# Kernel optimization log

Measured on AMD Instinct MI355X. Metric: run time of the kernel, lower is better.

Reference implementation:

```python
import jax, jax.numpy as jnp
import numpy as np

D_MODEL = 256
N_HEADS = 8
N_LEVELS = 3
N_POINTS = 4
HEAD_DIM = D_MODEL // N_HEADS
SPATIAL_SHAPES = [(80, 80), (40, 40), (20, 20)]
B = 16
LEN_Q = 300
N_TOTAL = sum(h * w for h, w in SPATIAL_SHAPES)  # 8400
N_LP = N_LEVELS * N_POINTS


def setup_inputs() -> dict:
    key = jax.random.key(0)
    ks = jax.random.split(key, 8)
    s = 0.02
    return {
        "query": jax.random.normal(ks[0], (B, LEN_Q, D_MODEL), jnp.float32),
        "reference_points": jax.random.uniform(ks[1], (B, LEN_Q, N_LEVELS, 2), jnp.float32),
        "input_flatten": jax.random.normal(ks[2], (B, N_TOTAL, D_MODEL), jnp.float32),
        "W_off": jax.random.normal(ks[3], (D_MODEL, N_HEADS * N_LP * 2), jnp.float32) * s,
        "b_off": jnp.zeros((N_HEADS * N_LP * 2,), jnp.float32),
        "W_attn": jax.random.normal(ks[4], (D_MODEL, N_HEADS * N_LP), jnp.float32) * s,
        "b_attn": jnp.zeros((N_HEADS * N_LP,), jnp.float32),
        "W_val": jax.random.normal(ks[5], (D_MODEL, D_MODEL), jnp.float32) * s,
        "b_val": jnp.zeros((D_MODEL,), jnp.float32),
        "W_out": jax.random.normal(ks[6], (D_MODEL, D_MODEL), jnp.float32) * s,
        "b_out": jnp.zeros((D_MODEL,), jnp.float32),
    }


def _ms_deform_core(value, sampling_locations, attention_weights):
    # value: (B, n_heads, head_dim, N_total); locations: (B, Lq, H, L, P, 2) in [0,1]
    Bq, Lq = sampling_locations.shape[0], sampling_locations.shape[1]
    BN = Bq * N_HEADS
    grids = 2.0 * sampling_locations - 1.0
    starts = np.cumsum([0] + [h * w for h, w in SPATIAL_SHAPES])
    sampled_levels = []
    for lid, (H, W) in enumerate(SPATIAL_SHAPES):
        val_l = value[..., starts[lid]:starts[lid + 1]]                    # (B,H,hd,HW)
        val_flat = val_l.reshape(BN, HEAD_DIM, H * W).transpose(0, 2, 1)   # (BN,HW,hd)
        g = grids[:, :, :, lid].transpose(0, 2, 1, 3, 4).reshape(BN, Lq, N_POINTS, 2)
        ix = ((g[..., 0] + 1.0) * W - 1.0) / 2.0
        iy = ((g[..., 1] + 1.0) * H - 1.0) / 2.0
        ix0 = jnp.floor(ix).astype(jnp.int32)
        iy0 = jnp.floor(iy).astype(jnp.int32)
        ix1 = ix0 + 1
        iy1 = iy0 + 1
        fx = (ix - ix0.astype(ix.dtype))[..., None]
        fy = (iy - iy0.astype(iy.dtype))[..., None]

        def corner(iyc, ixc):
            valid = ((ixc >= 0) & (ixc < W) & (iyc >= 0) & (iyc < H)).astype(val_flat.dtype)
            idx = (jnp.clip(iyc, 0, H - 1) * W + jnp.clip(ixc, 0, W - 1))
            idx = idx.reshape(BN, Lq * N_POINTS, 1)
            v = jnp.take_along_axis(val_flat, idx, axis=1)
            return v.reshape(BN, Lq, N_POINTS, HEAD_DIM) * valid[..., None]

        v00 = corner(iy0, ix0)
        v01 = corner(iy0, ix1)
        v10 = corner(iy1, ix0)
        v11 = corner(iy1, ix1)
        sampled = ((1 - fx) * (1 - fy)) * v00 + (fx * (1 - fy)) * v01 \
                + ((1 - fx) * fy) * v10 + (fx * fy) * v11
        sampled_levels.append(sampled.transpose(0, 3, 1, 2))               # (BN,hd,Lq,P)
    sv = jnp.stack(sampled_levels, axis=-2).reshape(BN, HEAD_DIM, Lq, N_LP)
    a = attention_weights.transpose(0, 2, 1, 3).reshape(BN, 1, Lq, N_LP)
    out = jnp.sum(sv * a, axis=-1)                                         # (BN,hd,Lq)
    return out.reshape(Bq, D_MODEL, Lq).transpose(0, 2, 1)                 # (B,Lq,D)


def reference(query, reference_points, input_flatten,
              W_off, b_off, W_attn, b_attn, W_val, b_val, W_out, b_out):
    Bq, Lq = query.shape[0], query.shape[1]
    value = input_flatten @ W_val + b_val
    value = value.reshape(Bq, -1, N_HEADS, HEAD_DIM).transpose(0, 2, 3, 1)  # (B,H,hd,N)
    off = (query @ W_off + b_off).reshape(Bq, Lq, N_HEADS, N_LEVELS, N_POINTS, 2)
    attn = jax.nn.softmax((query @ W_attn + b_attn).reshape(Bq, Lq, N_HEADS, N_LP), axis=-1)
    # offset normalizer is (W,H) per level (x first)
    norm = jnp.array([[w, h] for h, w in SPATIAL_SHAPES], jnp.float32)
    loc = reference_points[:, :, None, :, None, :] + off / norm[None, None, None, :, None, :]
    out = _ms_deform_core(value, loc, attn)
    return out @ W_out + b_out
```

## Files before the change

### kernel.cpp

```cpp
#include <hip/hip_runtime.h>
#include <hip/hip_bf16.h>

#define DM 256
#define NH 8
#define HD 32
#define NLV 3
#define NPT 4
#define NLP 12
#define BB 16
#define LQ 300
#define NT 8400
#define MROWS (BB * NT)
#define QROWS (BB * LQ)
#define KP2 72

typedef __bf16 bf16x8 __attribute__((ext_vector_type(8)));
typedef float  f32x16 __attribute__((ext_vector_type(16)));

__global__ void k_wt(const float* __restrict__ W_val,
                     const float* __restrict__ W_off,
                     const float* __restrict__ W_attn,
                     const float* __restrict__ W_out,
                     __hip_bfloat16* __restrict__ Wf,
                     __hip_bfloat16* __restrict__ Wf2,
                     __hip_bfloat16* __restrict__ Wf3)
{
    const int n = blockIdx.x;
    const int k = threadIdx.x;
    if (n < 256) {
        Wf[(size_t)(k >> 3) * 2048 + n * 8 + (k & 7)] =
            __float2bfloat16(W_val[(size_t)k * 256 + n]);
    } else if (n < 544) {
        const int n2 = n - 256;
        float v = (n2 < 192) ? W_off[(size_t)k * 192 + n2]
                             : W_attn[(size_t)k * 96 + (n2 - 192)];
        Wf2[(size_t)(k >> 3) * 2304 + n2 * 8 + (k & 7)] = __float2bfloat16(v);
    } else {
        const int n3 = n - 544;
        Wf3[(size_t)(k >> 3) * 2048 + n3 * 8 + (k & 7)] =
            __float2bfloat16(W_out[(size_t)k * 256 + n3]);
    }
}

__global__ __launch_bounds__(256) void k_mm1(
    const float* __restrict__ A,
    const __hip_bfloat16* __restrict__ Wf,
    const float* __restrict__ bval,
    __hip_bfloat16* __restrict__ V,
    const float* __restrict__ Q,
    const __hip_bfloat16* __restrict__ Wf2,
    const float* __restrict__ boff,
    const float* __restrict__ battn,
    float* __restrict__ off_out,
    float* __restrict__ attn_out)
{
    __shared__ __hip_bfloat16 As[2][32 * KP2];

    const int t    = threadIdx.x;
    const int wave = t >> 6;
    const int lane = t & 63;
    const int lm   = lane & 31;
    const int kh   = lane >> 5;
    const int lk   = kh * 8;
    const int ar   = t >> 3;
    const int ak   = (t & 7) * 8;

    if (blockIdx.x < MROWS / 32) {
        const int m0 = blockIdx.x * 32;

        f32x16 acc[2];
#pragma unroll
        for (int j = 0; j < 2; j++)
#pragma unroll
            for (int e = 0; e < 16; e++) acc[j][e] = 0.f;

        const __hip_bfloat16* wf0 = Wf + (size_t)(wave * 64 + lm) * 8 + kh * 2048;

        {
            const float* ap = A + (size_t)(m0 + ar) * 256 + ak;
            float4 a0 = *(const float4*)ap;
            float4 a1 = *(const float4*)(ap + 4);
            union { __hip_bfloat162 h2[4]; bf16x8 v; } ua;
            ua.h2[0] = __float22bfloat162_rn(make_float2(a0.x, a0.y));
            ua.h2[1] = __float22bfloat162_rn(make_float2(a0.z, a0.w));
            ua.h2[2] = __float22bfloat162_rn(make_float2(a1.x, a1.y));
            ua.h2[3] = __float22bfloat162_rn(make_float2(a1.z, a1.w));
            *(bf16x8*)(&As[0][ar * KP2 + ak]) = ua.v;
        }
        __syncthreads();

#pragma unroll
        for (int it = 0; it < 4; ++it) {
            const int buf = it & 1;
            float4 na0, na1;
            if (it < 3) {
                const float* ap = A + (size_t)(m0 + ar) * 256 + (it + 1) * 64 + ak;
                na0 = *(const float4*)ap;
                na1 = *(const float4*)(ap + 4);
            }
#pragma unroll
            for (int ks = 0; ks < 4; ++ks) {
                const int g = it * 4 + ks;
                bf16x8 af = *(const bf16x8*)(&As[buf][lm * KP2 + ks * 16 + lk]);
                bf16x8 b0 = *(const bf16x8*)(wf0 + (size_t)g * 4096);
                bf16x8 b1 = *(const bf16x8*)(wf0 + (size_t)g * 4096 + 256);
                acc[0] = __builtin_amdgcn_mfma_f32_32x32x16_bf16(af, b0, acc[0], 0, 0, 0);
                acc[1] = __builtin_amdgcn_mfma_f32_32x32x16_bf16(af, b1, acc[1], 0, 0, 0);
            }
            if (it < 3) {
                union { __hip_bfloat162 h2[4]; bf16x8 v; } ua;
                ua.h2[0] = __float22bfloat162_rn(make_float2(na0.x, na0.y));
                ua.h2[1] = __float22bfloat162_rn(make_float2(na0.z, na0.w));
                ua.h2[2] = __float22bfloat162_rn(make_float2(na1.x, na1.y));
                ua.h2[3] = __float22bfloat162_rn(make_float2(na1.z, na1.w));
                *(bf16x8*)(&As[buf ^ 1][ar * KP2 + ak]) = ua.v;
                __syncthreads();
            }
        }

#pragma unroll
        for (int j = 0; j < 2; j++) {
            const int n  = wave * 64 + j * 32 + lm;
            const float bn = bval[n];
            const int h  = n >> 5;
            const int d  = n & 31;
#pragma unroll
            for (int r = 0; r < 16; r++) {
                int rl = (r & 3) + 8 * (r >> 2) + 4 * kh;
                int m  = m0 + rl;
                int b  = m / NT;
                int pos = m - b * NT;
                V[((size_t)(b * NH + h) * NT + pos) * HD + d] =
                    __float2bfloat16(acc[j][r] + bn);
            }
        }
    } else {
        const int m0 = (blockIdx.x - MROWS / 32) * 32;

        f32x16 acc[3];
#pragma unroll
        for (int j = 0; j < 3; j++)
#pragma unroll
            for (int e = 0; e < 16; e++) acc[j][e] = 0.f;

        const __hip_bfloat16* wf0 = Wf2 + (size_t)(wave * 96 + lm) * 8 + kh * 2304;

        {
            const float* ap = Q + (size_t)(m0 + ar) * 256 + ak;
            float4 a0 = *(const float4*)ap;
            float4 a1 = *(const float4*)(ap + 4);
            union { __hip_bfloat162 h2[4]; bf16x8 v; } ua;
            ua.h2[0] = __float22bfloat162_rn(make_float2(a0.x, a0.y));
            ua.h2[1] = __float22bfloat162_rn(make_float2(a0.z, a0.w));
            ua.h2[2] = __float22bfloat162_rn(make_float2(a1.x, a1.y));
            ua.h2[3] = __float22bfloat162_rn(make_float2(a1.z, a1.w));
            *(bf16x8*)(&As[0][ar * KP2 + ak]) = ua.v;
        }
        __syncthreads();

#pragma unroll
        for (int it = 0; it < 4; ++it) {
            const int buf = it & 1;
            float4 na0, na1;
            if (it < 3) {
                const float* ap = Q + (size_t)(m0 + ar) * 256 + (it + 1) * 64 + ak;
                na0 = *(const float4*)ap;
                na1 = *(const float4*)(ap + 4);
            }
#pragma unroll
            for (int ks = 0; ks < 4; ++ks) {
                const int g = it * 4 + ks;
                bf16x8 af = *(const bf16x8*)(&As[buf][lm * KP2 + ks * 16 + lk]);
                if (wave < 3) {
#pragma unroll
                    for (int j = 0; j < 3; j++) {
                        bf16x8 bf = *(const bf16x8*)(wf0 + (size_t)g * 4608 + j * 256);
                        acc[j] = __builtin_amdgcn_mfma_f32_32x32x16_bf16(af, bf, acc[j], 0, 0, 0);
                    }
                }
            }
            if (it < 3) {
                union { __hip_bfloat162 h2[4]; bf16x8 v; } ua;
                ua.h2[0] = __float22bfloat162_rn(make_float2(na0.x, na0.y));
                ua.h2[1] = __float22bfloat162_rn(make_float2(na0.z, na0.w));
                ua.h2[2] = __float22bfloat162_rn(make_float2(na1.x, na1.y));
                ua.h2[3] = __float22bfloat162_rn(make_float2(na1.z, na1.w));
                *(bf16x8*)(&As[buf ^ 1][ar * KP2 + ak]) = ua.v;
                __syncthreads();
            }
        }

        if (wave < 3) {
#pragma unroll
            for (int j = 0; j < 3; j++) {
                const int n = wave * 96 + j * 32 + lm;
                const float bias_ = (n < 192) ? boff[n] : battn[n - 192];
#pragma unroll
                for (int r = 0; r < 16; r++) {
                    int rl = (r & 3) + 8 * (r >> 2) + 4 * kh;
                    int m  = m0 + rl;
                    float v = acc[j][r] + bias_;
                    if (n < 192) off_out[(size_t)m * 192 + n] = v;
                    else         attn_out[(size_t)m * 96 + (n - 192)] = v;
                }
            }
        }
    }
}

__global__ __launch_bounds__(256) void k_sample(
    const float* __restrict__ off_raw,
    const float* __restrict__ attn_raw,
    const float* __restrict__ refp,
    const __hip_bfloat16* __restrict__ V,
    __hip_bfloat16* __restrict__ sampled)
{
    const int t  = threadIdx.x;
    const int q2 = t >> 7;
    const int tq = t & 127;

    const int bid  = blockIdx.x;
    const int xcd  = bid & 7;
    const int slot = bid >> 3;
    const int hi   = (slot >= 150) ? 1 : 0;
    const int b    = xcd + (hi << 3);
    const int bq   = b * LQ + (slot - hi * 150) * 2 + q2;

    __shared__ float aw[2][96];
    __shared__ float wc[2][96][4];
    __shared__ int   ic[2][96][4];

    if (tq < 8) {
        float v[12];
        float mx = -1e30f;
#pragma unroll
        for (int i = 0; i < 12; i++) {
            v[i] = attn_raw[(size_t)bq * 96 + tq * 12 + i];
            mx = fmaxf(mx, v[i]);
        }
        float s = 0.f;
#pragma unroll
        for (int i = 0; i < 12; i++) { v[i] = expf(v[i] - mx); s += v[i]; }
        float inv = 1.f / s;
#pragma unroll
        for (int i = 0; i < 12; i++) aw[q2][tq * 12 + i] = v[i] * inv;
    }
    __syncthreads();

    if (tq < 96) {
        const float dims[3]  = {80.f, 40.f, 20.f};
        const int startsl[3] = {0, 6400, 8000};
        const int idiml[3]   = {80, 40, 20};
        int h = tq / 12, lp = tq - h * 12, l = lp >> 2, p = lp & 3;
        float ox = off_raw[(size_t)bq * 192 + ((h * 3 + l) * 4 + p) * 2 + 0];
        float oy = off_raw[(size_t)bq * 192 + ((h * 3 + l) * 4 + p) * 2 + 1];
        float rx = refp[(size_t)bq * 6 + l * 2 + 0];
        float ry = refp[(size_t)bq * 6 + l * 2 + 1];
        float D  = dims[l];
        float lx = rx + ox / D;
        float ly = ry + oy / D;
        float ix = lx * D - 0.5f;
        float iy = ly * D - 0.5f;
        const int Dl = idiml[l];
        const int st = startsl[l];

        float fix = floorf(ix), fiy = floorf(iy);
        int ix0 = (int)fix, iy0 = (int)fiy;
        int ix1 = ix0 + 1, iy1 = iy0 + 1;
        float fx = ix - fix, fy = iy - fiy;

        float mx0 = (ix0 >= 0 && ix0 < Dl) ? 1.f : 0.f;
        float mx1 = (ix1 >= 0 && ix1 < Dl) ? 1.f : 0.f;
        float my0 = (iy0 >= 0 && iy0 < Dl) ? 1.f : 0.f;
        float my1 = (iy1 >= 0 && iy1 < Dl) ? 1.f : 0.f;

        int cx0 = min(max(ix0, 0), Dl - 1);
        int cx1 = min(max(ix1, 0), Dl - 1);
        int cy0 = min(max(iy0, 0), Dl - 1);
        int cy1 = min(max(iy1, 0), Dl - 1);

        float a = aw[q2][tq];
        wc[q2][tq][0] = (1.f - fx) * (1.f - fy) * mx0 * my0 * a;
        wc[q2][tq][1] = fx * (1.f - fy) * mx1 * my0 * a;
        wc[q2][tq][2] = (1.f - fx) * fy * mx0 * my1 * a;
        wc[q2][tq][3] = fx * fy * mx1 * my1 * a;
        ic[q2][tq][0] = (st + cy0 * Dl + cx0) * HD;
        ic[q2][tq][1] = (st + cy0 * Dl + cx1) * HD;
        ic[q2][tq][2] = (st + cy1 * Dl + cx0) * HD;
        ic[q2][tq][3] = (st + cy1 * Dl + cx1) * HD;
    }
    __syncthreads();

    const int h  = tq >> 4;
    const int dp = (tq & 15) * 2;
    const __hip_bfloat16* vb = V + (size_t)(b * NH + h) * NT * HD + dp;

    float acc0 = 0.f, acc1 = 0.f;
#pragma unroll
    for (int lp = 0; lp < 12; lp++) {
        const int s = h * 12 + lp;
        float4 w4 = *(const float4*)(&wc[q2][s][0]);
        int4   i4 = *(const int4*)(&ic[q2][s][0]);
        float2 v00 = __bfloat1622float2(*(const __hip_bfloat162*)(vb + i4.x));
        float2 v01 = __bfloat1622float2(*(const __hip_bfloat162*)(vb + i4.y));
        float2 v10 = __bfloat1622float2(*(const __hip_bfloat162*)(vb + i4.z));
        float2 v11 = __bfloat1622float2(*(const __hip_bfloat162*)(vb + i4.w));
        acc0 = fmaf(w4.x, v00.x, fmaf(w4.y, v01.x, fmaf(w4.z, v10.x, fmaf(w4.w, v11.x, acc0))));
        acc1 = fmaf(w4.x, v00.y, fmaf(w4.y, v01.y, fmaf(w4.z, v10.y, fmaf(w4.w, v11.y, acc1))));
    }
    *(__hip_bfloat162*)(sampled + (size_t)bq * 256 + h * 32 + dp) =
        __float22bfloat162_rn(make_float2(acc0, acc1));
}

__global__ __launch_bounds__(256) void k_outproj(
    const __hip_bfloat16* __restrict__ A,
    const __hip_bfloat16* __restrict__ Wf3,
    const float* __restrict__ bias,
    float* __restrict__ out)
{
    __shared__ __hip_bfloat16 As[2][32 * KP2];

    const int t    = threadIdx.x;
    const int m0   = blockIdx.x * 32;
    const int wave = t >> 6;
    const int lane = t & 63;
    const int lm   = lane & 31;
    const int kh   = lane >> 5;
    const int lk   = kh * 8;
    const int ar   = t >> 3;
    const int ak   = (t & 7) * 8;

    f32x16 acc[2];
#pragma unroll
    for (int j = 0; j < 2; j++)
#pragma unroll
        for (int e = 0; e < 16; e++) acc[j][e] = 0.f;

    const __hip_bfloat16* wf0 = Wf3 + (size_t)(wave * 64 + lm) * 8 + kh * 2048;

    *(bf16x8*)(&As[0][ar * KP2 + ak]) =
        *(const bf16x8*)(A + (size_t)(m0 + ar) * 256 + ak);
    __syncthreads();

#pragma unroll
    for (int it = 0; it < 4; ++it) {
        const int buf = it & 1;
        bf16x8 na;
        if (it < 3)
            na = *(const bf16x8*)(A + (size_t)(m0 + ar) * 256 + (it + 1) * 64 + ak);
#pragma unroll
        for (int ks = 0; ks < 4; ++ks) {
            const int g = it * 4 + ks;
            bf16x8 af = *(const bf16x8*)(&As[buf][lm * KP2 + ks * 16 + lk]);
            bf16x8 b0 = *(const bf16x8*)(wf0 + (size_t)g * 4096);
            bf16x8 b1 = *(const bf16x8*)(wf0 + (size_t)g * 4096 + 256);
            acc[0] = __builtin_amdgcn_mfma_f32_32x32x16_bf16(af, b0, acc[0], 0, 0, 0);
            acc[1] = __builtin_amdgcn_mfma_f32_32x32x16_bf16(af, b1, acc[1], 0, 0, 0);
        }
        if (it < 3) {
            *(bf16x8*)(&As[buf ^ 1][ar * KP2 + ak]) = na;
            __syncthreads();
        }
    }

#pragma unroll
    for (int j = 0; j < 2; j++) {
        const int n = wave * 64 + j * 32 + lm;
        const float bn = bias[n];
#pragma unroll
        for (int r = 0; r < 16; r++) {
            int rl = (r & 3) + 8 * (r >> 2) + 4 * kh;
            int m  = m0 + rl;
            out[(size_t)m * 256 + n] = acc[j][r] + bn;
        }
    }
}

extern "C" void kernel_launch(void* const* d_in, const int* in_sizes, int n_in,
                              void* d_out, int out_size, void* d_ws, size_t ws_size,
                              hipStream_t stream) {
    const float* query  = (const float*)d_in[0];
    const float* refp   = (const float*)d_in[1];
    const float* inputf = (const float*)d_in[2];
    const float* W_off  = (const float*)d_in[3];
    const float* b_off  = (const float*)d_in[4];
    const float* W_attn = (const float*)d_in[5];
    const float* b_attn = (const float*)d_in[6];
    const float* W_val  = (const float*)d_in[7];
    const float* b_val  = (const float*)d_in[8];
    const float* W_out  = (const float*)d_in[9];
    const float* b_out  = (const float*)d_in[10];
    float* out = (float*)d_out;

    char* ws = (char*)d_ws;
    __hip_bfloat16* value   = (__hip_bfloat16*)ws;
    float* off_raw          = (float*)(ws + 68812800);
    float* attn_raw         = (float*)(ws + 72499200);
    __hip_bfloat16* sampled = (__hip_bfloat16*)(ws + 74342400);
    __hip_bfloat16* Wf      = (__hip_bfloat16*)(ws + 76800000);
    __hip_bfloat16* Wf2     = (__hip_bfloat16*)(ws + 76931072);
    __hip_bfloat16* Wf3     = (__hip_bfloat16*)(ws + 77078528);

    k_wt<<<800, 256, 0, stream>>>(W_val, W_off, W_attn, W_out, Wf, Wf2, Wf3);
    k_mm1<<<MROWS / 32 + QROWS / 32, 256, 0, stream>>>(
        inputf, Wf, b_val, value, query, Wf2, b_off, b_attn, off_raw, attn_raw);
    k_sample<<<QROWS / 2, 256, 0, stream>>>(off_raw, attn_raw, refp, value, sampled);
    k_outproj<<<QROWS / 32, 256, 0, stream>>>(sampled, Wf3, b_out, out);
}
```

Baseline: 267.4 us.

## Drop LDS staging in GEMMs; load MFMA operands directly with register prefetch

Reworks the three MFMA GEMM kernels so each wave loads its A and weight fragments straight from global memory into registers, using a 4-deep (or 2-deep) rotating prefetch. This removes the shared-memory double buffer and its __syncthreads. Weights are now stored row-major (n, k) to match the per-lane fragment loads, and the idle fourth wave in the query projection now exits early. The cost is that each of the four waves loads the same A tile separately (4x redundant A reads, served from L1/L2), uses more registers, and issues strided row loads for A.

```diff
diff --git a/kernel.cpp b/kernel.cpp
--- a/kernel.cpp
+++ b/kernel.cpp
@@ -12,7 +12,6 @@
 #define NT 8400
 #define MROWS (BB * NT)
 #define QROWS (BB * LQ)
-#define KP2 72
 
 typedef __bf16 bf16x8 __attribute__((ext_vector_type(8)));
 typedef float  f32x16 __attribute__((ext_vector_type(16)));
@@ -28,17 +27,15 @@
     const int n = blockIdx.x;
     const int k = threadIdx.x;
     if (n < 256) {
-        Wf[(size_t)(k >> 3) * 2048 + n * 8 + (k & 7)] =
-            __float2bfloat16(W_val[(size_t)k * 256 + n]);
+        Wf[(size_t)n * 256 + k] = __float2bfloat16(W_val[(size_t)k * 256 + n]);
     } else if (n < 544) {
         const int n2 = n - 256;
         float v = (n2 < 192) ? W_off[(size_t)k * 192 + n2]
                              : W_attn[(size_t)k * 96 + (n2 - 192)];
-        Wf2[(size_t)(k >> 3) * 2304 + n2 * 8 + (k & 7)] = __float2bfloat16(v);
+        Wf2[(size_t)n2 * 256 + k] = __float2bfloat16(v);
     } else {
         const int n3 = n - 544;
-        Wf3[(size_t)(k >> 3) * 2048 + n3 * 8 + (k & 7)] =
-            __float2bfloat16(W_out[(size_t)k * 256 + n3]);
+        Wf3[(size_t)n3 * 256 + k] = __float2bfloat16(W_out[(size_t)k * 256 + n3]);
     }
 }
 
@@ -54,16 +51,11 @@
     float* __restrict__ off_out,
     float* __restrict__ attn_out)
 {
-    __shared__ __hip_bfloat16 As[2][32 * KP2];
-
     const int t    = threadIdx.x;
     const int wave = t >> 6;
     const int lane = t & 63;
     const int lm   = lane & 31;
     const int kh   = lane >> 5;
-    const int lk   = kh * 8;
-    const int ar   = t >> 3;
-    const int ak   = (t & 7) * 8;
 
     if (blockIdx.x < MROWS / 32) {
         const int m0 = blockIdx.x * 32;
@@ -74,48 +66,37 @@
 #pragma unroll
             for (int e = 0; e < 16; e++) acc[j][e] = 0.f;
 
-        const __hip_bfloat16* wf0 = Wf + (size_t)(wave * 64 + lm) * 8 + kh * 2048;
-
-        {
-            const float* ap = A + (size_t)(m0 + ar) * 256 + ak;
-            float4 a0 = *(const float4*)ap;
-            float4 a1 = *(const float4*)(ap + 4);
+        const float* ap = A + (size_t)(m0 + lm) * 256 + kh * 8;
+        const __hip_bfloat16* w0p = Wf + (size_t)(wave * 64 + lm) * 256 + kh * 8;
+        const __hip_bfloat16* w1p = w0p + 32 * 256;
+
+        float4 pa0[4], pa1[4];
+        bf16x8 pw0[4], pw1[4];
+#pragma unroll
+        for (int g = 0; g < 4; ++g) {
+            pa0[g] = *(const float4*)(ap + g * 16);
+            pa1[g] = *(const float4*)(ap + g * 16 + 4);
+            pw0[g] = *(const bf16x8*)(w0p + g * 16);
+            pw1[g] = *(const bf16x8*)(w1p + g * 16);
+        }
+#pragma unroll
+        for (int g = 0; g < 16; ++g) {
+            const int s = g & 3;
+            float4 a0 = pa0[s], a1 = pa1[s];
+            bf16x8 b0 = pw0[s], b1 = pw1[s];
+            if (g < 12) {
+                pa0[s] = *(const float4*)(ap + (g + 4) * 16);
+                pa1[s] = *(const float4*)(ap + (g + 4) * 16 + 4);
+                pw0[s] = *(const bf16x8*)(w0p + (g + 4) * 16);
+                pw1[s] = *(const bf16x8*)(w1p + (g + 4) * 16);
+            }
             union { __hip_bfloat162 h2[4]; bf16x8 v; } ua;
             ua.h2[0] = __float22bfloat162_rn(make_float2(a0.x, a0.y));
             ua.h2[1] = __float22bfloat162_rn(make_float2(a0.z, a0.w));
             ua.h2[2] = __float22bfloat162_rn(make_float2(a1.x, a1.y));
             ua.h2[3] = __float22bfloat162_rn(make_float2(a1.z, a1.w));
-            *(bf16x8*)(&As[0][ar * KP2 + ak]) = ua.v;
-        }
-        __syncthreads();
-
-#pragma unroll
-        for (int it = 0; it < 4; ++it) {
-            const int buf = it & 1;
-            float4 na0, na1;
-            if (it < 3) {
-                const float* ap = A + (size_t)(m0 + ar) * 256 + (it + 1) * 64 + ak;
-                na0 = *(const float4*)ap;
-                na1 = *(const float4*)(ap + 4);
-            }
-#pragma unroll
-            for (int ks = 0; ks < 4; ++ks) {
-                const int g = it * 4 + ks;
-                bf16x8 af = *(const bf16x8*)(&As[buf][lm * KP2 + ks * 16 + lk]);
-                bf16x8 b0 = *(const bf16x8*)(wf0 + (size_t)g * 4096);
-                bf16x8 b1 = *(const bf16x8*)(wf0 + (size_t)g * 4096 + 256);
-                acc[0] = __builtin_amdgcn_mfma_f32_32x32x16_bf16(af, b0, acc[0], 0, 0, 0);
-                acc[1] = __builtin_amdgcn_mfma_f32_32x32x16_bf16(af, b1, acc[1], 0, 0, 0);
-            }
-            if (it < 3) {
-                union { __hip_bfloat162 h2[4]; bf16x8 v; } ua;
-                ua.h2[0] = __float22bfloat162_rn(make_float2(na0.x, na0.y));
-                ua.h2[1] = __float22bfloat162_rn(make_float2(na0.z, na0.w));
-                ua.h2[2] = __float22bfloat162_rn(make_float2(na1.x, na1.y));
-                ua.h2[3] = __float22bfloat162_rn(make_float2(na1.z, na1.w));
-                *(bf16x8*)(&As[buf ^ 1][ar * KP2 + ak]) = ua.v;
-                __syncthreads();
-            }
+            acc[0] = __builtin_amdgcn_mfma_f32_32x32x16_bf16(ua.v, b0, acc[0], 0, 0, 0);
+            acc[1] = __builtin_amdgcn_mfma_f32_32x32x16_bf16(ua.v, b1, acc[1], 0, 0, 0);
         }
 
 #pragma unroll
@@ -136,6 +117,7 @@
         }
     } else {
         const int m0 = (blockIdx.x - MROWS / 32) * 32;
+        if (wave >= 3) return;
 
         f32x16 acc[3];
 #pragma unroll
@@ -143,66 +125,54 @@
 #pragma unroll
             for (int e = 0; e < 16; e++) acc[j][e] = 0.f;
 
-        const __hip_bfloat16* wf0 = Wf2 + (size_t)(wave * 96 + lm) * 8 + kh * 2304;
-
-        {
-            const float* ap = Q + (size_t)(m0 + ar) * 256 + ak;
-            float4 a0 = *(const float4*)ap;
-            float4 a1 = *(const float4*)(ap + 4);
+        const float* ap = Q + (size_t)(m0 + lm) * 256 + kh * 8;
+        const __hip_bfloat16* w0p = Wf2 + (size_t)(wave * 96 + lm) * 256 + kh * 8;
+        const __hip_bfloat16* w1p = w0p + 32 * 256;
+        const __hip_bfloat16* w2p = w0p + 64 * 256;
+
+        float4 pa0[2], pa1[2];
+        bf16x8 pw0[2], pw1[2], pw2[2];
+#pragma unroll
+        for (int g = 0; g < 2; ++g) {
+            pa0[g] = *(const float4*)(ap + g * 16);
+            pa1[g] = *(const float4*)(ap + g * 16 + 4);
+            pw0[g] = *(const bf16x8*)(w0p + g * 16);
+            pw1[g] = *(const bf16x8*)(w1p + g * 16);
+            pw2[g] = *(const bf16x8*)(w2p + g * 16);
+        }
+#pragma unroll
+        for (int g = 0; g < 16; ++g) {
+            const int s = g & 1;
+            float4 a0 = pa0[s], a1 = pa1[s];
+            bf16x8 b0 = pw0[s], b1 = pw1[s], b2 = pw2[s];
+            if (g < 14) {
+                pa0[s] = *(const float4*)(ap + (g + 2) * 16);
+                pa1[s] = *(const float4*)(ap + (g + 2) * 16 + 4);
+                pw0[s] = *(const bf16x8*)(w0p + (g + 2) * 16);
+                pw1[s] = *(const bf16x8*)(w1p + (g + 2) * 16);
+                pw2[s] = *(const bf16x8*)(w2p + (g + 2) * 16);
+            }
             union { __hip_bfloat162 h2[4]; bf16x8 v; } ua;
             ua.h2[0] = __float22bfloat162_rn(make_float2(a0.x, a0.y));
             ua.h2[1] = __float22bfloat162_rn(make_float2(a0.z, a0.w));
             ua.h2[2] = __float22bfloat162_rn(make_float2(a1.x, a1.y));
             ua.h2[3] = __float22bfloat162_rn(make_float2(a1.z, a1.w));
-            *(bf16x8*)(&As[0][ar * KP2 + ak]) = ua.v;
-        }
-        __syncthreads();
-
-#pragma unroll
-        for (int it = 0; it < 4; ++it) {
-            const int buf = it & 1;
-            float4 na0, na1;
-            if (it < 3) {
-                const float* ap = Q + (size_t)(m0 + ar) * 256 + (it + 1) * 64 + ak;
-                na0 = *(const float4*)ap;
-                na1 = *(const float4*)(ap + 4);
-            }
-#pragma unroll
-            for (int ks = 0; ks < 4; ++ks) {
-                const int g = it * 4 + ks;
-                bf16x8 af = *(const bf16x8*)(&As[buf][lm * KP2 + ks * 16 + lk]);
-                if (wave < 3) {
-#pragma unroll
-                    for (int j = 0; j < 3; j++) {
-                        bf16x8 bf = *(const bf16x8*)(wf0 + (size_t)g * 4608 + j * 256);
-                        acc[j] = __builtin_amdgcn_mfma_f32_32x32x16_bf16(af, bf, acc[j], 0, 0, 0);
-                    }
-                }
-            }
-            if (it < 3) {
-                union { __hip_bfloat162 h2[4]; bf16x8 v; } ua;
-                ua.h2[0] = __float22bfloat162_rn(make_float2(na0.x, na0.y));
-                ua.h2[1] = __float22bfloat162_rn(make_float2(na0.z, na0.w));
-                ua.h2[2] = __float22bfloat162_rn(make_float2(na1.x, na1.y));
-                ua.h2[3] = __float22bfloat162_rn(make_float2(na1.z, na1.w));
-                *(bf16x8*)(&As[buf ^ 1][ar * KP2 + ak]) = ua.v;
-                __syncthreads();
-            }
-        }
-
-        if (wave < 3) {
-#pragma unroll
-            for (int j = 0; j < 3; j++) {
-                const int n = wave * 96 + j * 32 + lm;
-                const float bias_ = (n < 192) ? boff[n] : battn[n - 192];
-#pragma unroll
-                for (int r = 0; r < 16; r++) {
-                    int rl = (r & 3) + 8 * (r >> 2) + 4 * kh;
-                    int m  = m0 + rl;
-                    float v = acc[j][r] + bias_;
-                    if (n < 192) off_out[(size_t)m * 192 + n] = v;
-                    else         attn_out[(size_t)m * 96 + (n - 192)] = v;
-                }
+            acc[0] = __builtin_amdgcn_mfma_f32_32x32x16_bf16(ua.v, b0, acc[0], 0, 0, 0);
+            acc[1] = __builtin_amdgcn_mfma_f32_32x32x16_bf16(ua.v, b1, acc[1], 0, 0, 0);
+            acc[2] = __builtin_amdgcn_mfma_f32_32x32x16_bf16(ua.v, b2, acc[2], 0, 0, 0);
+        }
+
+#pragma unroll
+        for (int j = 0; j < 3; j++) {
+            const int n = wave * 96 + j * 32 + lm;
+            const float bias_ = (n < 192) ? boff[n] : battn[n - 192];
+#pragma unroll
+            for (int r = 0; r < 16; r++) {
+                int rl = (r & 3) + 8 * (r >> 2) + 4 * kh;
+                int m  = m0 + rl;
+                float v = acc[j][r] + bias_;
+                if (n < 192) off_out[(size_t)m * 192 + n] = v;
+                else         attn_out[(size_t)m * 96 + (n - 192)] = v;
             }
         }
     }
@@ -318,17 +288,12 @@
     const float* __restrict__ bias,
     float* __restrict__ out)
 {
-    __shared__ __hip_bfloat16 As[2][32 * KP2];
-
     const int t    = threadIdx.x;
     const int m0   = blockIdx.x * 32;
     const int wave = t >> 6;
     const int lane = t & 63;
     const int lm   = lane & 31;
     const int kh   = lane >> 5;
-    const int lk   = kh * 8;
-    const int ar   = t >> 3;
-    const int ak   = (t & 7) * 8;
 
     f32x16 acc[2];
 #pragma unroll
@@ -336,31 +301,28 @@
 #pragma unroll
         for (int e = 0; e < 16; e++) acc[j][e] = 0.f;
 
-    const __hip_bfloat16* wf0 = Wf3 + (size_t)(wave * 64 + lm) * 8 + kh * 2048;
-
-    *(bf16x8*)(&As[0][ar * KP2 + ak]) =
-        *(const bf16x8*)(A + (size_t)(m0 + ar) * 256 + ak);
-    __syncthreads();
-
-#pragma unroll
-    for (int it = 0; it < 4; ++it) {
-        const int buf = it & 1;
-        bf16x8 na;
-        if (it < 3)
-            na = *(const bf16x8*)(A + (size_t)(m0 + ar) * 256 + (it + 1) * 64 + ak);
-#pragma unroll
-        for (int ks = 0; ks < 4; ++ks) {
-            const int g = it * 4 + ks;
-            bf16x8 af = *(const bf16x8*)(&As[buf][lm * KP2 + ks * 16 + lk]);
-            bf16x8 b0 = *(const bf16x8*)(wf0 + (size_t)g * 4096);
-            bf16x8 b1 = *(const bf16x8*)(wf0 + (size_t)g * 4096 + 256);
-            acc[0] = __builtin_amdgcn_mfma_f32_32x32x16_bf16(af, b0, acc[0], 0, 0, 0);
-            acc[1] = __builtin_amdgcn_mfma_f32_32x32x16_bf16(af, b1, acc[1], 0, 0, 0);
-        }
-        if (it < 3) {
-            *(bf16x8*)(&As[buf ^ 1][ar * KP2 + ak]) = na;
-            __syncthreads();
-        }
+    const __hip_bfloat16* ap  = A + (size_t)(m0 + lm) * 256 + kh * 8;
+    const __hip_bfloat16* w0p = Wf3 + (size_t)(wave * 64 + lm) * 256 + kh * 8;
+    const __hip_bfloat16* w1p = w0p + 32 * 256;
+
+    bf16x8 pa[4], pw0[4], pw1[4];
+#pragma unroll
+    for (int g = 0; g < 4; ++g) {
+        pa[g]  = *(const bf16x8*)(ap + g * 16);
+        pw0[g] = *(const bf16x8*)(w0p + g * 16);
+        pw1[g] = *(const bf16x8*)(w1p + g * 16);
+    }
+#pragma unroll
+    for (int g = 0; g < 16; ++g) {
+        const int s = g & 3;
+        bf16x8 af = pa[s], b0 = pw0[s], b1 = pw1[s];
+        if (g < 12) {
+            pa[s]  = *(const bf16x8*)(ap + (g + 4) * 16);
+            pw0[s] = *(const bf16x8*)(w0p + (g + 4) * 16);
+            pw1[s] = *(const bf16x8*)(w1p + (g + 4) * 16);
+        }
+        acc[0] = __builtin_amdgcn_mfma_f32_32x32x16_bf16(af, b0, acc[0], 0, 0, 0);
+        acc[1] = __builtin_amdgcn_mfma_f32_32x32x16_bf16(af, b1, acc[1], 0, 0, 0);
     }
 
 #pragma unroll
```

New measurement: 365.0 us. 36.5% more time.
